# Kernel optimization log

Hardware: AMD Instinct MI355X
Metric: run time of the kernel (lower is better)

Reference implementation:

```python
import jax, jax.numpy as jnp
import numpy as np

B, IN_DIM, OUT_DIM, CB_DIM = 8192, 4096, 4096, 1  # L = OUT_DIM codebooks, 2 codewords each


def setup_inputs() -> dict:
    key = jax.random.key(0)
    k_x, k_w, k_e = jax.random.split(key, 3)
    x = jax.random.normal(k_x, (B, IN_DIM), dtype=jnp.float32)
    W = jax.random.normal(k_w, (IN_DIM, OUT_DIM), dtype=jnp.float32) * (1.0 / np.sqrt(IN_DIM))
    b = jnp.zeros((OUT_DIM,), dtype=jnp.float32)
    # embedding.data.uniform_(-1/2, 1/2)
    embedding = jax.random.uniform(k_e, (OUT_DIM, 2, CB_DIM), dtype=jnp.float32, minval=-0.5, maxval=0.5)
    return {"x": x, "W": W, "b": b, "embedding": embedding}


def reference(x, W, b, embedding):
    L, d = embedding.shape[0], embedding.shape[2]
    # backbone (ToyNet modeled as a single Linear)
    z_e = x @ W + b                                    # [B, L*d]
    z = z_e.reshape(-1, L, d)                          # [B, L, d]
    # squared distance to each of the 2 codewords per codebook
    dist = jnp.sum((z[:, :, None, :] - embedding[None]) ** 2, axis=-1)  # [B, L, 2]
    indices = jnp.argmin(dist, axis=-1)                # [B, L] in {0,1}
    # gather the selected codeword per (batch, codebook)
    quantized = embedding[jnp.arange(L)[None, :], indices]  # [B, L, d]
    quantized = quantized.reshape(-1, L * d)           # [B, L*d]
    # straight-through estimator
    quantized_st = z_e + jax.lax.stop_gradient(quantized - z_e)
    return indices, embedding, quantized_st, z_e
```

## Files before the change

### kernel.cpp

```cpp
#include <hip/hip_runtime.h>

#define B_ROWS  8192
#define IN_DIM  4096
#define OUT_DIM 4096

#define BM 64
#define BN 64
#define BK 16
#define TILES (IN_DIM / BK)
#define LDS_A 68
#define LDS_B 68

__global__ __launch_bounds__(256) void vq_fused_gemm(
    const float* __restrict__ X, const float* __restrict__ Wm,
    const float* __restrict__ bvec, const float* __restrict__ emb,
    float* __restrict__ out_idx, float* __restrict__ out_q, float* __restrict__ out_ze)
{
    __shared__ float As[BK * LDS_A];
    __shared__ float Bs[BK * LDS_B];

    const int tid  = threadIdx.x;
    const int tx   = tid & 15;
    const int ty   = tid >> 4;
    const int brow = blockIdx.y * BM;
    const int bcol = blockIdx.x * BN;

    const int a_row = tid >> 2;
    const int a_k   = (tid & 3) << 2;
    const int b_k   = tid >> 4;
    const int b_col = (tid & 15) << 2;

    const float* Aptr = X  + (size_t)(brow + a_row) * IN_DIM + a_k;
    const float* Bptr = Wm + (size_t)b_k * OUT_DIM + bcol + b_col;

    float acc_tot[4][4];
    float acc_blk[4][4];
    #pragma unroll
    for (int i = 0; i < 4; ++i)
        #pragma unroll
        for (int j = 0; j < 4; ++j) { acc_tot[i][j] = 0.0f; acc_blk[i][j] = 0.0f; }

    for (int t = 0; t < TILES; ++t) {
        const int k0 = t * BK;
        float4 av = *reinterpret_cast<const float4*>(Aptr + k0);
        float4 bv = *reinterpret_cast<const float4*>(Bptr + (size_t)k0 * OUT_DIM);
        __syncthreads();
        As[(a_k + 0) * LDS_A + a_row] = av.x;
        As[(a_k + 1) * LDS_A + a_row] = av.y;
        As[(a_k + 2) * LDS_A + a_row] = av.z;
        As[(a_k + 3) * LDS_A + a_row] = av.w;
        *reinterpret_cast<float4*>(&Bs[b_k * LDS_B + b_col]) = bv;
        __syncthreads();

        #pragma unroll
        for (int kk = 0; kk < BK; ++kk) {
            float4 af = *reinterpret_cast<const float4*>(&As[kk * LDS_A + ty * 4]);
            float4 bf = *reinterpret_cast<const float4*>(&Bs[kk * LDS_B + tx * 4]);
            acc_blk[0][0] = fmaf(af.x, bf.x, acc_blk[0][0]);
            acc_blk[0][1] = fmaf(af.x, bf.y, acc_blk[0][1]);
            acc_blk[0][2] = fmaf(af.x, bf.z, acc_blk[0][2]);
            acc_blk[0][3] = fmaf(af.x, bf.w, acc_blk[0][3]);
            acc_blk[1][0] = fmaf(af.y, bf.x, acc_blk[1][0]);
            acc_blk[1][1] = fmaf(af.y, bf.y, acc_blk[1][1]);
            acc_blk[1][2] = fmaf(af.y, bf.z, acc_blk[1][2]);
            acc_blk[1][3] = fmaf(af.y, bf.w, acc_blk[1][3]);
            acc_blk[2][0] = fmaf(af.z, bf.x, acc_blk[2][0]);
            acc_blk[2][1] = fmaf(af.z, bf.y, acc_blk[2][1]);
            acc_blk[2][2] = fmaf(af.z, bf.z, acc_blk[2][2]);
            acc_blk[2][3] = fmaf(af.z, bf.w, acc_blk[2][3]);
            acc_blk[3][0] = fmaf(af.w, bf.x, acc_blk[3][0]);
            acc_blk[3][1] = fmaf(af.w, bf.y, acc_blk[3][1]);
            acc_blk[3][2] = fmaf(af.w, bf.z, acc_blk[3][2]);
            acc_blk[3][3] = fmaf(af.w, bf.w, acc_blk[3][3]);
        }

        const int done = t + 1;
        if ((done & 31) == 0) {
            #pragma unroll
            for (int i = 0; i < 4; ++i)
                #pragma unroll
                for (int j = 0; j < 4; ++j) {
                    acc_tot[i][j] = acc_tot[i][j] + acc_blk[i][j];
                    acc_blk[i][j] = 0.0f;
                }
        }
    }

    const int c0 = bcol + tx * 4;
    float e0c[4], e1c[4], bb[4];
    #pragma unroll
    for (int j = 0; j < 4; ++j) {
        e0c[j] = emb[2 * (c0 + j) + 0];
        e1c[j] = emb[2 * (c0 + j) + 1];
        bb[j]  = bvec[c0 + j];
    }

    #pragma unroll
    for (int i = 0; i < 4; ++i) {
        const int r = brow + ty * 4 + i;
        float4 vidx, vq, vz;
        float* pi = (float*)&vidx;
        float* pq = (float*)&vq;
        float* pz = (float*)&vz;
        #pragma unroll
        for (int j = 0; j < 4; ++j) {
            float zb    = acc_tot[i][j] + bb[j];
            float diff0 = zb - e0c[j];
            float diff1 = zb - e1c[j];
            float d0    = diff0 * diff0;
            float d1    = diff1 * diff1;
            int   idx   = (d1 < d0) ? 1 : 0;
            float qf    = idx ? e1c[j] : e0c[j];
            pi[j] = (float)idx;
            pq[j] = zb + (qf - zb);
            pz[j] = zb;
        }
        size_t off = (size_t)r * OUT_DIM + c0;
        *reinterpret_cast<float4*>(&out_idx[off]) = vidx;
        *reinterpret_cast<float4*>(&out_q[off])   = vq;
        *reinterpret_cast<float4*>(&out_ze[off])  = vz;
    }
}

__global__ void copy_emb(const float* __restrict__ emb, float* __restrict__ out, int n)
{
    int i = blockIdx.x * blockDim.x + threadIdx.x;
    if (i < n) out[i] = emb[i];
}

extern "C" void kernel_launch(void* const* d_in, const int* in_sizes, int n_in,
                              void* d_out, int out_size, void* d_ws, size_t ws_size,
                              hipStream_t stream)
{
    const float* X   = (const float*)d_in[0];
    const float* W   = (const float*)d_in[1];
    const float* b   = (const float*)d_in[2];
    const float* emb = (const float*)d_in[3];

    float* out = (float*)d_out;
    const size_t n_big = (size_t)B_ROWS * OUT_DIM;
    float* out_idx = out;
    float* out_emb = out + n_big;
    float* out_q   = out_emb + (size_t)OUT_DIM * 2;
    float* out_ze  = out_q + n_big;

    dim3 grid(OUT_DIM / BN, B_ROWS / BM);
    vq_fused_gemm<<<grid, dim3(256), 0, stream>>>(X, W, b, emb, out_idx, out_q, out_ze);

    int nemb = OUT_DIM * 2;
    copy_emb<<<(nemb + 255) / 256, 256, 0, stream>>>(emb, out_emb, nemb);
}
```

Before: 3.497 ms.

## Enlarge GEMM block tile to 128x128 with 8x8 per-thread micro-tile

Doubles the block tile in both dimensions and gives each thread a 2x2 grid of 4x4 sub-tiles, so each thread computes 64 outputs from four LDS float4 loads per k-step instead of 16. Global loads become two float4 per thread per operand, and the epilogue is restructured to match. This raises arithmetic intensity and cuts LDS and global traffic per FMA. In exchange it uses many more registers (128 accumulators with the split-sum scheme) with launch bounds asking for 2 blocks per CU, which risks spills or lower occupancy.

```diff
diff --git a/kernel.cpp b/kernel.cpp
--- a/kernel.cpp
+++ b/kernel.cpp
@@ -4,20 +4,20 @@
 #define IN_DIM  4096
 #define OUT_DIM 4096
 
-#define BM 64
-#define BN 64
+#define BM 128
+#define BN 128
 #define BK 16
 #define TILES (IN_DIM / BK)
-#define LDS_A 68
-#define LDS_B 68
+#define PADA 132
+#define PADB 132
 
-__global__ __launch_bounds__(256) void vq_fused_gemm(
+__global__ __launch_bounds__(256, 2) void vq_fused_gemm(
     const float* __restrict__ X, const float* __restrict__ Wm,
     const float* __restrict__ bvec, const float* __restrict__ emb,
     float* __restrict__ out_idx, float* __restrict__ out_q, float* __restrict__ out_ze)
 {
-    __shared__ float As[BK * LDS_A];
-    __shared__ float Bs[BK * LDS_B];
+    __shared__ float As[BK * PADA];
+    __shared__ float Bs[BK * PADB];
 
     const int tid  = threadIdx.x;
     const int tx   = tid & 15;
@@ -25,101 +25,124 @@
     const int brow = blockIdx.y * BM;
     const int bcol = blockIdx.x * BN;
 
-    const int a_row = tid >> 2;
-    const int a_k   = (tid & 3) << 2;
+    const int a_row = tid >> 1;
+    const int a_k   = (tid & 1) << 3;
     const int b_k   = tid >> 4;
-    const int b_col = (tid & 15) << 2;
+    const int b_col = (tid & 15) << 3;
 
     const float* Aptr = X  + (size_t)(brow + a_row) * IN_DIM + a_k;
     const float* Bptr = Wm + (size_t)b_k * OUT_DIM + bcol + b_col;
 
-    float acc_tot[4][4];
-    float acc_blk[4][4];
+    float acc_tot[2][2][4][4];
+    float acc_blk[2][2][4][4];
     #pragma unroll
-    for (int i = 0; i < 4; ++i)
+    for (int im = 0; im < 2; ++im)
         #pragma unroll
-        for (int j = 0; j < 4; ++j) { acc_tot[i][j] = 0.0f; acc_blk[i][j] = 0.0f; }
+        for (int jm = 0; jm < 2; ++jm)
+            #pragma unroll
+            for (int i = 0; i < 4; ++i)
+                #pragma unroll
+                for (int j = 0; j < 4; ++j) {
+                    acc_tot[im][jm][i][j] = 0.0f;
+                    acc_blk[im][jm][i][j] = 0.0f;
+                }
 
     for (int t = 0; t < TILES; ++t) {
         const int k0 = t * BK;
-        float4 av = *reinterpret_cast<const float4*>(Aptr + k0);
-        float4 bv = *reinterpret_cast<const float4*>(Bptr + (size_t)k0 * OUT_DIM);
+        float4 av0 = *reinterpret_cast<const float4*>(Aptr + k0);
+        float4 av1 = *reinterpret_cast<const float4*>(Aptr + k0 + 4);
+        float4 bv0 = *reinterpret_cast<const float4*>(Bptr + (size_t)k0 * OUT_DIM);
+        float4 bv1 = *reinterpret_cast<const float4*>(Bptr + (size_t)k0 * OUT_DIM + 4);
         __syncthreads();
-        As[(a_k + 0) * LDS_A + a_row] = av.x;
-        As[(a_k + 1) * LDS_A + a_row] = av.y;
-        As[(a_k + 2) * LDS_A + a_row] = av.z;
-        As[(a_k + 3) * LDS_A + a_row] = av.w;
-        *reinterpret_cast<float4*>(&Bs[b_k * LDS_B + b_col]) = bv;
+        As[(a_k + 0) * PADA + a_row] = av0.x;
+        As[(a_k + 1) * PADA + a_row] = av0.y;
+        As[(a_k + 2) * PADA + a_row] = av0.z;
+        As[(a_k + 3) * PADA + a_row] = av0.w;
+        As[(a_k + 4) * PADA + a_row] = av1.x;
+        As[(a_k + 5) * PADA + a_row] = av1.y;
+        As[(a_k + 6) * PADA + a_row] = av1.z;
+        As[(a_k + 7) * PADA + a_row] = av1.w;
+        *reinterpret_cast<float4*>(&Bs[b_k * PADB + b_col])     = bv0;
+        *reinterpret_cast<float4*>(&Bs[b_k * PADB + b_col + 4]) = bv1;
         __syncthreads();
 
         #pragma unroll
         for (int kk = 0; kk < BK; ++kk) {
-            float4 af = *reinterpret_cast<const float4*>(&As[kk * LDS_A + ty * 4]);
-            float4 bf = *reinterpret_cast<const float4*>(&Bs[kk * LDS_B + tx * 4]);
-            acc_blk[0][0] = fmaf(af.x, bf.x, acc_blk[0][0]);
-            acc_blk[0][1] = fmaf(af.x, bf.y, acc_blk[0][1]);
-            acc_blk[0][2] = fmaf(af.x, bf.z, acc_blk[0][2]);
-            acc_blk[0][3] = fmaf(af.x, bf.w, acc_blk[0][3]);
-            acc_blk[1][0] = fmaf(af.y, bf.x, acc_blk[1][0]);
-            acc_blk[1][1] = fmaf(af.y, bf.y, acc_blk[1][1]);
-            acc_blk[1][2] = fmaf(af.y, bf.z, acc_blk[1][2]);
-            acc_blk[1][3] = fmaf(af.y, bf.w, acc_blk[1][3]);
-            acc_blk[2][0] = fmaf(af.z, bf.x, acc_blk[2][0]);
-            acc_blk[2][1] = fmaf(af.z, bf.y, acc_blk[2][1]);
-            acc_blk[2][2] = fmaf(af.z, bf.z, acc_blk[2][2]);
-            acc_blk[2][3] = fmaf(af.z, bf.w, acc_blk[2][3]);
-            acc_blk[3][0] = fmaf(af.w, bf.x, acc_blk[3][0]);
-            acc_blk[3][1] = fmaf(af.w, bf.y, acc_blk[3][1]);
-            acc_blk[3][2] = fmaf(af.w, bf.z, acc_blk[3][2]);
-            acc_blk[3][3] = fmaf(af.w, bf.w, acc_blk[3][3]);
+            float4 a0 = *reinterpret_cast<const float4*>(&As[kk * PADA + ty * 4]);
+            float4 a1 = *reinterpret_cast<const float4*>(&As[kk * PADA + 64 + ty * 4]);
+            float4 b0 = *reinterpret_cast<const float4*>(&Bs[kk * PADB + tx * 4]);
+            float4 b1 = *reinterpret_cast<const float4*>(&Bs[kk * PADB + 64 + tx * 4]);
+            const float* ap[2] = { (const float*)&a0, (const float*)&a1 };
+            const float* bp[2] = { (const float*)&b0, (const float*)&b1 };
+            #pragma unroll
+            for (int im = 0; im < 2; ++im)
+                #pragma unroll
+                for (int jm = 0; jm < 2; ++jm)
+                    #pragma unroll
+                    for (int i = 0; i < 4; ++i)
+                        #pragma unroll
+                        for (int j = 0; j < 4; ++j)
+                            acc_blk[im][jm][i][j] =
+                                fmaf(ap[im][i], bp[jm][j], acc_blk[im][jm][i][j]);
         }
 
-        const int done = t + 1;
-        if ((done & 31) == 0) {
+        if (((t + 1) & 31) == 0) {
             #pragma unroll
-            for (int i = 0; i < 4; ++i)
+            for (int im = 0; im < 2; ++im)
                 #pragma unroll
-                for (int j = 0; j < 4; ++j) {
-                    acc_tot[i][j] = acc_tot[i][j] + acc_blk[i][j];
-                    acc_blk[i][j] = 0.0f;
-                }
+                for (int jm = 0; jm < 2; ++jm)
+                    #pragma unroll
+                    for (int i = 0; i < 4; ++i)
+                        #pragma unroll
+                        for (int j = 0; j < 4; ++j) {
+                            acc_tot[im][jm][i][j] += acc_blk[im][jm][i][j];
+                            acc_blk[im][jm][i][j] = 0.0f;
+                        }
         }
     }
 
-    const int c0 = bcol + tx * 4;
-    float e0c[4], e1c[4], bb[4];
+    float e0c[2][4], e1c[2][4], bb[2][4];
     #pragma unroll
-    for (int j = 0; j < 4; ++j) {
-        e0c[j] = emb[2 * (c0 + j) + 0];
-        e1c[j] = emb[2 * (c0 + j) + 1];
-        bb[j]  = bvec[c0 + j];
+    for (int jm = 0; jm < 2; ++jm) {
+        const int cb = bcol + jm * 64 + tx * 4;
+        #pragma unroll
+        for (int j = 0; j < 4; ++j) {
+            e0c[jm][j] = emb[2 * (cb + j) + 0];
+            e1c[jm][j] = emb[2 * (cb + j) + 1];
+            bb[jm][j]  = bvec[cb + j];
+        }
     }
 
     #pragma unroll
-    for (int i = 0; i < 4; ++i) {
-        const int r = brow + ty * 4 + i;
-        float4 vidx, vq, vz;
-        float* pi = (float*)&vidx;
-        float* pq = (float*)&vq;
-        float* pz = (float*)&vz;
+    for (int im = 0; im < 2; ++im)
         #pragma unroll
-        for (int j = 0; j < 4; ++j) {
-            float zb    = acc_tot[i][j] + bb[j];
-            float diff0 = zb - e0c[j];
-            float diff1 = zb - e1c[j];
-            float d0    = diff0 * diff0;
-            float d1    = diff1 * diff1;
-            int   idx   = (d1 < d0) ? 1 : 0;
-            float qf    = idx ? e1c[j] : e0c[j];
-            pi[j] = (float)idx;
-            pq[j] = zb + (qf - zb);
-            pz[j] = zb;
+        for (int i = 0; i < 4; ++i) {
+            const int r = brow + im * 64 + ty * 4 + i;
+            #pragma unroll
+            for (int jm = 0; jm < 2; ++jm) {
+                float4 vidx, vq, vz;
+                float* pi = (float*)&vidx;
+                float* pq = (float*)&vq;
+                float* pz = (float*)&vz;
+                #pragma unroll
+                for (int j = 0; j < 4; ++j) {
+                    float zb    = acc_tot[im][jm][i][j] + bb[jm][j];
+                    float diff0 = zb - e0c[jm][j];
+                    float diff1 = zb - e1c[jm][j];
+                    float d0    = diff0 * diff0;
+                    float d1    = diff1 * diff1;
+                    int   idx   = (d1 < d0) ? 1 : 0;
+                    float qf    = idx ? e1c[jm][j] : e0c[jm][j];
+                    pi[j] = (float)idx;
+                    pq[j] = zb + (qf - zb);
+                    pz[j] = zb;
+                }
+                size_t off = (size_t)r * OUT_DIM + bcol + jm * 64 + tx * 4;
+                *reinterpret_cast<float4*>(&out_idx[off]) = vidx;
+                *reinterpret_cast<float4*>(&out_q[off])   = vq;
+                *reinterpret_cast<float4*>(&out_ze[off])  = vz;
+            }
         }
-        size_t off = (size_t)r * OUT_DIM + c0;
-        *reinterpret_cast<float4*>(&out_idx[off]) = vidx;
-        *reinterpret_cast<float4*>(&out_q[off])   = vq;
-        *reinterpret_cast<float4*>(&out_ze[off])  = vz;
-    }
 }
 
 __global__ void copy_emb(const float* __restrict__ emb, float* __restrict__ out, int n)
```

Result: faster. 3.386 ms (-3.2%).
